# Kernel optimization log

Hardware: AMD Instinct MI355X
Metric: run time of the kernel (lower is better)

The kernel has to match this reference:

```python
import jax, jax.numpy as jnp
import numpy as np

HEADS = 8
LOCAL_ATTN_CTX = 64  # local_attn_ctx
BLOCKSIZE = 32       # only used for divisibility assert in original


def _strided_transpose(x, local_attn_ctx):
    # [n, t, e] -> group seq into (bT_ctx, local) blocks and transpose them
    n, t, e = x.shape
    bT_ctx = t // local_attn_ctx
    x = x.reshape(n, bT_ctx, local_attn_ctx, e)
    x = jnp.transpose(x, (0, 2, 1, 3))
    return x.reshape(n, t, e)


def setup_inputs() -> dict:
    key = jax.random.key(0)
    kq, kk, kv = jax.random.split(key, 3)
    shape = (4, 4096, 512)  # [batch, n_ctx, embd]
    return {
        "q": jax.random.normal(kq, shape, dtype=jnp.float32),
        "k": jax.random.normal(kk, shape, dtype=jnp.float32),
        "v": jax.random.normal(kv, shape, dtype=jnp.float32),
    }


def reference(q, k, v):
    n_ctx = q.shape[1]
    bT_ctx = n_ctx // LOCAL_ATTN_CTX
    assert bT_ctx % BLOCKSIZE == 0
    # strided permutation of the sequence axis
    qs = _strided_transpose(q, LOCAL_ATTN_CTX)
    ks = _strided_transpose(k, LOCAL_ATTN_CTX)
    vs = _strided_transpose(v, LOCAL_ATTN_CTX)
    n_state = q.shape[-1] // HEADS
    scale = np.float32(1.0 / np.sqrt(n_state))
    # full attention over the permuted sequence (as in the torch impl)
    w = jnp.einsum('nte,nse->nts', qs, ks)          # [n, t, t]
    w = jax.nn.softmax(w * scale, axis=-1)
    a = jnp.einsum('nts,nse->nte', w, vs)           # [n, t, e]
    # inverse strided regrouping
    n, t, e = a.shape
    a = a.reshape(n, LOCAL_ATTN_CTX, bT_ctx, e)
    a = jnp.transpose(a, (0, 2, 1, 3))
    return a.reshape(n, t, e)
```

## Files before the change

### kernel.cpp

```cpp
#include <hip/hip_runtime.h>


typedef _Float16 half8 __attribute__((ext_vector_type(8)));
typedef float f32x16 __attribute__((ext_vector_type(16)));
typedef float f32x4v __attribute__((ext_vector_type(4)));

#define B 4
#define S 4096
#define D 512
#define QT 64
#define KT 64
#define NT 64
#define NELEM (B * S * D)

#define QSCALE 0.18033688011112042f
#define M0 20.0f

__global__ __launch_bounds__(256) void cvt(const float* __restrict__ k,
                                           const float* __restrict__ v,
                                           _Float16* __restrict__ k16,
                                           _Float16* __restrict__ v16) {
  __shared__ half8 tile[32][65];
  const int tid = threadIdx.x;
  int bx = blockIdx.x;
  if (bx < 512) {
    const int b = bx >> 7;
    const int t0 = (bx & 127) * 32;
#pragma unroll
    for (int p = 0; p < 8; ++p) {
      const int tl = p * 4 + (tid >> 6);
      const int dcl = tid & 63;
      const float* src = k + ((size_t)(b * S + t0 + tl) * D) + dcl * 8;
      f32x4v x = *(const f32x4v*)src;
      f32x4v y = *(const f32x4v*)(src + 4);
      half8 h;
      h[0] = (_Float16)x[0]; h[1] = (_Float16)x[1]; h[2] = (_Float16)x[2]; h[3] = (_Float16)x[3];
      h[4] = (_Float16)y[0]; h[5] = (_Float16)y[1]; h[6] = (_Float16)y[2]; h[7] = (_Float16)y[3];
      tile[tl][dcl] = h;
    }
    __syncthreads();
#pragma unroll
    for (int p = 0; p < 8; ++p) {
      const int dcw = p * 8 + (tid >> 5);
      const int tw = tid & 31;
      ((half8*)k16)[(size_t)(b * 64 + dcw) * S + t0 + tw] = tile[tw][dcw];
    }
  } else {
    bx -= 512;
    const int i = bx * 256 + tid;
    const int dq = i & 127;
    const int bt8 = i >> 7;
    const int b = bt8 >> 9, t8 = bt8 & 511;
    const float* src = v + ((size_t)(b * S + t8 * 8) * D) + dq * 4;
    f32x4v r[8];
#pragma unroll
    for (int j = 0; j < 8; ++j) r[j] = *(const f32x4v*)(src + (size_t)j * D);
    half8* dst = (half8*)v16 + ((size_t)bt8 * 512 + dq * 4);
#pragma unroll
    for (int c = 0; c < 4; ++c) {
      half8 h;
#pragma unroll
      for (int j = 0; j < 8; ++j) h[j] = (_Float16)r[j][c];
      dst[c] = h;
    }
  }
}

#define KBUF_H 32768
#define PBUF_H 5120
#define KBUF_OFF 0
#define PBUF_OFF (2 * KBUF_H * 2)
#define LBUF_OFF (PBUF_OFF + 2 * PBUF_H * 2)
#define SMEM_SZ  (LBUF_OFF + 512)

__global__ __launch_bounds__(512)
__attribute__((amdgpu_waves_per_eu(2, 2)))
void attn(const float* __restrict__ q,
          const _Float16* __restrict__ k16,
          const _Float16* __restrict__ v16,
          float* __restrict__ out) {
  __shared__ __align__(16) char smem[SMEM_SZ];
  _Float16* Kbuf = (_Float16*)(smem + KBUF_OFF);
  _Float16* Pbuf = (_Float16*)(smem + PBUF_OFF);
  float*    Lbuf = (float*)(smem + LBUF_OFF);

  const int tid = threadIdx.x;
  const int w = tid >> 6, lane = tid & 63;
  const int m32 = lane & 31, hi = lane >> 5;

  const int bx = blockIdx.x;
  const int xc = bx & 7, rr0 = bx >> 3;
  const int b = xc >> 1;
  const int qt = ((xc & 1) << 5) + rr0;

  if (w < 4) {
    const int rg = w & 1, kh = (w >> 1) & 1;
    const int qrow0 = qt * QT + rg * 32;

#pragma unroll
    for (int i = 0; i < 16; ++i) {
      const int dc = w * 16 + i;
      const _Float16* g = k16 + ((size_t)(b * 64 + dc) * S + lane) * 8;
      __builtin_amdgcn_global_load_lds(
          (const __attribute__((address_space(1))) void*)g,
          (__attribute__((address_space(3))) void*)&Kbuf[dc * 512], 16, 0, 0);
    }

    half8 qf[32];
    {
      const float* qb = q + ((size_t)(b * S + qrow0 + m32) * D) + hi * 8;
#pragma unroll
      for (int ks = 0; ks < 32; ++ks) {
        f32x4v x = *(const f32x4v*)(qb + ks * 16);
        f32x4v y = *(const f32x4v*)(qb + ks * 16 + 4);
        half8 h;
        h[0] = (_Float16)(x[0] * QSCALE); h[1] = (_Float16)(x[1] * QSCALE);
        h[2] = (_Float16)(x[2] * QSCALE); h[3] = (_Float16)(x[3] * QSCALE);
        h[4] = (_Float16)(y[0] * QSCALE); h[5] = (_Float16)(y[1] * QSCALE);
        h[6] = (_Float16)(y[2] * QSCALE); h[7] = (_Float16)(y[3] * QSCALE);
        qf[ks] = h;
      }
    }
    float lacc[16];
#pragma unroll
    for (int r = 0; r < 16; ++r) lacc[r] = 0.f;

    for (int t = 0; t <= NT; ++t) {
      asm volatile("s_waitcnt vmcnt(0) lgkmcnt(0)" ::: "memory");
      __builtin_amdgcn_s_barrier();
      asm volatile("" ::: "memory");
      if (t == NT) break;
      if (t + 1 < NT) {
#pragma unroll
        for (int i = 0; i < 16; ++i) {
          const int dc = w * 16 + i;
          const _Float16* g = k16 + ((size_t)(b * 64 + dc) * S + (t + 1) * KT + lane) * 8;
          __builtin_amdgcn_global_load_lds(
              (const __attribute__((address_space(1))) void*)g,
              (__attribute__((address_space(3))) void*)&Kbuf[((t + 1) & 1) * KBUF_H + dc * 512],
              16, 0, 0);
        }
      }
      f32x16 sa0 = {}, sa1 = {};
      const _Float16* kb0 = &Kbuf[(t & 1) * KBUF_H + (hi * 64 + kh * 32 + m32) * 8];
      __builtin_amdgcn_s_setprio(1);
#pragma unroll
      for (int ks = 0; ks < 32; ks += 2) {
        half8 bf0 = *(const half8*)(kb0 + ks * 1024);
        half8 bf1 = *(const half8*)(kb0 + (ks + 1) * 1024);
        sa0 = __builtin_amdgcn_mfma_f32_32x32x16_f16(qf[ks], bf0, sa0, 0, 0, 0);
        sa1 = __builtin_amdgcn_mfma_f32_32x32x16_f16(qf[ks + 1], bf1, sa1, 0, 0, 0);
      }
      __builtin_amdgcn_s_setprio(0);
      _Float16* pq = &Pbuf[(t & 1) * PBUF_H + (kh * 2 + rg) * 1280];
#pragma unroll
      for (int r = 0; r < 16; ++r) {
        float p = __builtin_amdgcn_exp2f(fminf((sa0[r] + sa1[r]) - M0, 15.0f));
        lacc[r] += p;
        const int row = (r & 3) + 8 * (r >> 2) + 4 * hi;
        pq[row * 40 + m32] = (_Float16)p;
      }
    }

#pragma unroll
    for (int r = 0; r < 16; ++r) {
      float vv = lacc[r];
      vv += __shfl_xor(vv, 1);  vv += __shfl_xor(vv, 2);
      vv += __shfl_xor(vv, 4);  vv += __shfl_xor(vv, 8);
      vv += __shfl_xor(vv, 16);
      lacc[r] = vv;
    }
    if (m32 == 0) {
#pragma unroll
      for (int r = 0; r < 16; ++r) {
        const int row = (r & 3) + 8 * (r >> 2) + 4 * hi;
        Lbuf[kh * 64 + rg * 32 + row] = lacc[r];
      }
    }
    asm volatile("s_waitcnt lgkmcnt(0)" ::: "memory");
    __builtin_amdgcn_s_barrier();
  } else {
    const int j = w - 4;
    f32x16 o[2][4];
#pragma unroll
    for (int rt = 0; rt < 2; ++rt)
#pragma unroll
      for (int dn = 0; dn < 4; ++dn) o[rt][dn] = (f32x16){};

    half8 vf[2][4];
    const _Float16* vb0 = v16 + ((size_t)(b * 512 + hi) * 512 + j * 128 + m32) * 8;

    for (int t = 0; t <= NT; ++t) {
      asm volatile("" ::: "memory");
      __builtin_amdgcn_s_barrier();
      asm volatile("" ::: "memory");
      if (t == 0) {
#pragma unroll
        for (int ks = 0; ks < 4; ++ks)
          vf[0][ks] = *(const half8*)(vb0 + ((size_t)(ks * 2) * 512) * 8);
        continue;
      }
      const int u = t - 1;

      const _Float16* pb = &Pbuf[(u & 1) * PBUF_H];
      half8 pf[2][4];
#pragma unroll
      for (int rt = 0; rt < 2; ++rt)
#pragma unroll
        for (int ks = 0; ks < 4; ++ks)
          pf[rt][ks] = *(const half8*)(pb + ((ks >> 1) * 2 + rt) * 1280 + m32 * 40 +
                                       (ks & 1) * 16 + hi * 8);

      const _Float16* vb = vb0 + (size_t)u * 8 * 512 * 8;
#pragma unroll
      for (int dn = 0; dn < 4; ++dn) {
        if (dn < 3) {
#pragma unroll
          for (int ks = 0; ks < 4; ++ks)
            vf[(dn + 1) & 1][ks] =
                *(const half8*)(vb + ((size_t)(ks * 2) * 512 + (dn + 1) * 32) * 8);
        } else if (u + 1 < NT) {
#pragma unroll
          for (int ks = 0; ks < 4; ++ks)
            vf[0][ks] = *(const half8*)(vb + ((size_t)(ks * 2 + 8) * 512) * 8);
        }
        __builtin_amdgcn_s_setprio(1);
#pragma unroll
        for (int ks = 0; ks < 4; ++ks) {
          o[0][dn] = __builtin_amdgcn_mfma_f32_32x32x16_f16(pf[0][ks], vf[dn & 1][ks],
                                                            o[0][dn], 0, 0, 0);
          o[1][dn] = __builtin_amdgcn_mfma_f32_32x32x16_f16(pf[1][ks], vf[dn & 1][ks],
                                                            o[1][dn], 0, 0, 0);
        }
        __builtin_amdgcn_s_setprio(0);
      }
    }

    asm volatile("" ::: "memory");
    __builtin_amdgcn_s_barrier();
    asm volatile("" ::: "memory");
    float* ob = out + (size_t)(b * S + qt * QT) * D + j * 128;
#pragma unroll
    for (int rt = 0; rt < 2; ++rt)
#pragma unroll
      for (int r = 0; r < 16; ++r) {
        const int row = rt * 32 + (r & 3) + 8 * (r >> 2) + 4 * hi;
        const float lt = Lbuf[row] + Lbuf[64 + row];
        const float inv = 1.0f / lt;
#pragma unroll
        for (int dn = 0; dn < 4; ++dn)
          ob[(size_t)row * D + dn * 32 + m32] = o[rt][dn][r] * inv;
      }
  }
}

extern "C" void kernel_launch(void* const* d_in, const int* in_sizes, int n_in,
                              void* d_out, int out_size, void* d_ws, size_t ws_size,
                              hipStream_t stream) {
  const float* q = (const float*)d_in[0];
  const float* k = (const float*)d_in[1];
  const float* v = (const float*)d_in[2];
  float* out = (float*)d_out;

  _Float16* k16 = (_Float16*)d_ws;
  _Float16* v16 = k16 + NELEM;

  cvt<<<1536, 256, 0, stream>>>(k, v, k16, v16);
  attn<<<256, 512, 0, stream>>>(q, k16, v16, out);
}
```

Measured before the change: 285.7 us.

## Load K fragments directly from global into registers instead of staging via LDS

The QK^T producer waves stop staging K tiles into a double-buffered 128 KB LDS region with global_load_lds. They now read their K fragments straight from global memory into a two-slot register ring, prefetching the next group of eight fragments while the current group's MFMAs run. This removes the LDS traffic and large shared allocation, and drops the vmcnt wait from the per-tile barrier. In exchange, each wave issues redundant global loads, since K is no longer shared across waves through LDS. It also uses more VGPRs and relies on the compiler placing vmcnt waits well.

```diff
diff --git a/kernel.cpp b/kernel.cpp
--- a/kernel.cpp
+++ b/kernel.cpp
@@ -66,11 +66,9 @@
   }
 }
 
-#define KBUF_H 32768
 #define PBUF_H 5120
-#define KBUF_OFF 0
-#define PBUF_OFF (2 * KBUF_H * 2)
-#define LBUF_OFF (PBUF_OFF + 2 * PBUF_H * 2)
+#define PBUF_OFF 0
+#define LBUF_OFF (2 * PBUF_H * 2)
 #define SMEM_SZ  (LBUF_OFF + 512)
 
 __global__ __launch_bounds__(512)
@@ -80,7 +78,6 @@
           const _Float16* __restrict__ v16,
           float* __restrict__ out) {
   __shared__ __align__(16) char smem[SMEM_SZ];
-  _Float16* Kbuf = (_Float16*)(smem + KBUF_OFF);
   _Float16* Pbuf = (_Float16*)(smem + PBUF_OFF);
   float*    Lbuf = (float*)(smem + LBUF_OFF);
 
@@ -97,14 +94,11 @@
     const int rg = w & 1, kh = (w >> 1) & 1;
     const int qrow0 = qt * QT + rg * 32;
 
-#pragma unroll
-    for (int i = 0; i < 16; ++i) {
-      const int dc = w * 16 + i;
-      const _Float16* g = k16 + ((size_t)(b * 64 + dc) * S + lane) * 8;
-      __builtin_amdgcn_global_load_lds(
-          (const __attribute__((address_space(1))) void*)g,
-          (__attribute__((address_space(3))) void*)&Kbuf[dc * 512], 16, 0, 0);
-    }
+    const _Float16* kb = k16 + ((size_t)(b * 64 + hi) * S + kh * 32 + m32) * 8;
+    half8 kg[2][8];
+#pragma unroll
+    for (int i = 0; i < 8; ++i)
+      kg[0][i] = *(const half8*)(kb + (size_t)i * (S * 16));
 
     half8 qf[32];
     {
@@ -126,32 +120,31 @@
     for (int r = 0; r < 16; ++r) lacc[r] = 0.f;
 
     for (int t = 0; t <= NT; ++t) {
-      asm volatile("s_waitcnt vmcnt(0) lgkmcnt(0)" ::: "memory");
+      asm volatile("s_waitcnt lgkmcnt(0)" ::: "memory");
       __builtin_amdgcn_s_barrier();
       asm volatile("" ::: "memory");
       if (t == NT) break;
-      if (t + 1 < NT) {
-#pragma unroll
-        for (int i = 0; i < 16; ++i) {
-          const int dc = w * 16 + i;
-          const _Float16* g = k16 + ((size_t)(b * 64 + dc) * S + (t + 1) * KT + lane) * 8;
-          __builtin_amdgcn_global_load_lds(
-              (const __attribute__((address_space(1))) void*)g,
-              (__attribute__((address_space(3))) void*)&Kbuf[((t + 1) & 1) * KBUF_H + dc * 512],
-              16, 0, 0);
-        }
-      }
       f32x16 sa0 = {}, sa1 = {};
-      const _Float16* kb0 = &Kbuf[(t & 1) * KBUF_H + (hi * 64 + kh * 32 + m32) * 8];
-      __builtin_amdgcn_s_setprio(1);
-#pragma unroll
-      for (int ks = 0; ks < 32; ks += 2) {
-        half8 bf0 = *(const half8*)(kb0 + ks * 1024);
-        half8 bf1 = *(const half8*)(kb0 + (ks + 1) * 1024);
-        sa0 = __builtin_amdgcn_mfma_f32_32x32x16_f16(qf[ks], bf0, sa0, 0, 0, 0);
-        sa1 = __builtin_amdgcn_mfma_f32_32x32x16_f16(qf[ks + 1], bf1, sa1, 0, 0, 0);
-      }
-      __builtin_amdgcn_s_setprio(0);
+#pragma unroll
+      for (int g = 0; g < 4; ++g) {
+        if (g < 3) {
+#pragma unroll
+          for (int i = 0; i < 8; ++i)
+            kg[(g + 1) & 1][i] = *(const half8*)(kb + (size_t)((g + 1) * 8 + i) * (S * 16) +
+                                                 (size_t)t * 512);
+        } else if (t + 1 < NT) {
+#pragma unroll
+          for (int i = 0; i < 8; ++i)
+            kg[0][i] = *(const half8*)(kb + (size_t)i * (S * 16) + (size_t)(t + 1) * 512);
+        }
+        __builtin_amdgcn_s_setprio(1);
+#pragma unroll
+        for (int i = 0; i < 8; i += 2) {
+          sa0 = __builtin_amdgcn_mfma_f32_32x32x16_f16(qf[g * 8 + i], kg[g & 1][i], sa0, 0, 0, 0);
+          sa1 = __builtin_amdgcn_mfma_f32_32x32x16_f16(qf[g * 8 + i + 1], kg[g & 1][i + 1], sa1, 0, 0, 0);
+        }
+        __builtin_amdgcn_s_setprio(0);
+      }
       _Float16* pq = &Pbuf[(t & 1) * PBUF_H + (kh * 2 + rg) * 1280];
 #pragma unroll
       for (int r = 0; r < 16; ++r) {
```

Result: no change. 289.8 us (+1.4%).
